# Performance work log

Hardware: AMD Instinct MI355X
Metric: run time of the kernel (lower is better)

The kernel has to match this reference:

```python
import jax, jax.numpy as jnp
from jax import lax
import numpy as np

D_MODEL = 1024
EXPAND = 2
D_INNER = D_MODEL * EXPAND
D_STATE = 16
D_CONV = 4
DECAY = 0.95
LN_EPS = 1e-5


def setup_inputs() -> dict:
    key = jax.random.key(0)
    ks = jax.random.split(key, 9)
    b, s = 4, 2048
    scale = 1.0 / np.sqrt(D_MODEL)
    inner_scale = 1.0 / np.sqrt(D_INNER)
    return {
        "x": jax.random.normal(ks[0], (b, s, D_MODEL), dtype=jnp.float32),
        "W_in": jax.random.normal(ks[1], (2 * D_INNER, D_MODEL), dtype=jnp.float32) * scale,
        "conv_w": jax.random.normal(ks[2], (D_INNER, 1, D_CONV), dtype=jnp.float32) * 0.5,
        "conv_b": jax.random.normal(ks[3], (D_INNER,), dtype=jnp.float32) * 0.1,
        "W_x": jax.random.normal(ks[4], (2 * D_STATE, D_INNER), dtype=jnp.float32) * inner_scale,
        "B_log": jax.random.normal(ks[5], (D_INNER, D_STATE), dtype=jnp.float32) * 0.05,  # xavier-ish small
        "W_out": jax.random.normal(ks[6], (D_MODEL, D_INNER), dtype=jnp.float32) * inner_scale,
        "ln_g": jnp.ones((D_MODEL,), dtype=jnp.float32),
        "ln_b": jnp.zeros((D_MODEL,), dtype=jnp.float32),
    }


def _ssm_block(x, W_in, conv_w, conv_b, W_x, B_log, W_out, ln_g, ln_b):
    b, s, _ = x.shape
    d_inner = W_in.shape[0] // 2
    d_conv = conv_w.shape[-1]

    # input projection and gate split
    xz = jnp.einsum('bsd,ed->bse', x, W_in)            # [b, s, 2*d_inner]
    x_inner, z = jnp.split(xz, 2, axis=-1)             # each [b, s, d_inner]

    # causal depthwise conv (left pad d_conv-1, output length s)
    xc = jnp.transpose(x_inner, (0, 2, 1))             # [b, d_inner, s]
    conv = lax.conv_general_dilated(
        xc, conv_w, window_strides=(1,), padding=[(d_conv - 1, 0)],
        feature_group_count=d_inner)
    conv = conv + conv_b[None, :, None]
    x_conv = jax.nn.silu(jnp.transpose(conv, (0, 2, 1)))  # [b, s, d_inner]

    # selective parameters; s_B is produced but unused in the original math
    sp = jnp.einsum('bsd,nd->bsn', x_conv, W_x)        # [b, s, 2*d_state]
    _s_B, s_C = jnp.split(sp, 2, axis=-1)              # each [b, s, d_state]

    B = jnp.exp(B_log)                                  # [d_inner, d_state]

    # state_t = 0.95*state_{t-1} + B * x_t  factorizes as  state = B[d,n]*h[b,t,d]
    # with h_t = 0.95*h_{t-1} + x_conv_t ; scan over time with [b, d_inner] carry.
    def step(h, xt):
        h = DECAY * h + xt
        return h, h

    h0 = jnp.zeros((b, d_inner), dtype=x.dtype)
    _, h = lax.scan(step, h0, jnp.swapaxes(x_conv, 0, 1))  # [s, b, d_inner]
    h = jnp.swapaxes(h, 0, 1)                              # [b, s, d_inner]

    # output_t[b,d] = sum_n state[b,d,n]*s_C[b,t,n] = h[b,t,d] * (s_C @ B^T)[b,t,d]
    y = h * jnp.einsum('bsn,dn->bsd', s_C, B)
    y = y * jax.nn.silu(z)
    y = jnp.einsum('bsd,od->bso', y, W_out)            # [b, s, d_model]

    resid = x + y
    mu = jnp.mean(resid, axis=-1, keepdims=True)
    var = jnp.var(resid, axis=-1, keepdims=True)
    return (resid - mu) * lax.rsqrt(var + LN_EPS) * ln_g + ln_b


def reference(x, W_in, conv_w, conv_b, W_x, B_log, W_out, ln_g, ln_b):
    return _ssm_block(x, W_in, conv_w, conv_b, W_x, B_log, W_out, ln_g, ln_b)
```

## Files before the change

### kernel.cpp

```cpp
#include <hip/hip_runtime.h>
#include <hip/hip_bf16.h>
#include <stdint.h>

#define DM   1024
#define DI   2048
#define NST  16
#define BSZ  4
#define SLEN 2048
#define MROWS (BSZ*SLEN)
#define CHUNK 32
#define NCH  (SLEN/CHUNK)
#define DECAYF 0.95f
#define MB (size_t)1048576

typedef _Float16 f16;
typedef __attribute__((ext_vector_type(2))) _Float16 f16x2;
typedef __attribute__((ext_vector_type(4))) _Float16 f16x4;
typedef __attribute__((ext_vector_type(8))) _Float16 f16x8;
typedef __attribute__((ext_vector_type(4))) float f32x4;

__device__ __forceinline__ float silu_f(float v) { return v / (1.f + __expf(-v)); }

__device__ __forceinline__ void gload16(const f16* lds, const f16* g) {
  __builtin_amdgcn_global_load_lds((const __attribute__((address_space(1))) void*)g,
                                   (__attribute__((address_space(3))) void*)lds, 16, 0, 0);
}

#define NX4  (MROWS * DM / 4)
#define NWI4 (2 * DI * DM / 4)
#define NWO4 (DM * DI / 4)
#define NWX4 (NST * DI / 4)
#define NE4  (NST * DI / 4)
__global__ __launch_bounds__(256) void cvt_all(
    const float* __restrict__ x, const float* __restrict__ wi, const float* __restrict__ wo,
    const float* __restrict__ Wx, const float* __restrict__ B_log,
    f16* __restrict__ A1, f16* __restrict__ B1, f16* __restrict__ W2,
    f16* __restrict__ WxC, f16* __restrict__ expBT)
{
  int i = blockIdx.x * 256 + threadIdx.x;
  if (i < NX4 + NWI4 + NWO4 + NWX4) {
    const float* src; f16* dst; int j;
    if (i < NX4)                     { src = x;  dst = A1; j = i; }
    else if (i < NX4 + NWI4)         { src = wi; dst = B1; j = i - NX4; }
    else if (i < NX4 + NWI4 + NWO4)  { src = wo; dst = W2; j = i - NX4 - NWI4; }
    else                             { src = Wx + (size_t)NST * DI; dst = WxC; j = i - NX4 - NWI4 - NWO4; }
    float4 v = ((const float4*)src)[j];
    f16x4 o = {(f16)v.x, (f16)v.y, (f16)v.z, (f16)v.w};
    ((f16x4*)dst)[j] = o;
  } else {
    int j = i - NX4 - NWI4 - NWO4 - NWX4;
    int base = j * 4;
    int n = base >> 11, d = base & (DI - 1);
    f16x4 o = {(f16)__expf(B_log[(d + 0) * NST + n]), (f16)__expf(B_log[(d + 1) * NST + n]),
               (f16)__expf(B_log[(d + 2) * NST + n]), (f16)__expf(B_log[(d + 3) * NST + n])};
    ((f16x4*)expBT)[j] = o;
  }
}

#define G1K 1024

__device__ __forceinline__ void stage_t(const f16* __restrict__ mat, int matBase,
                                        int kt, f16* ldsDst, int tid) {
  #pragma unroll
  for (int q = 0; q < 2; ++q) {
    int c = q * 512 + tid;
    int row = c >> 2, p = c & 3;
    int su = p ^ ((row >> 1) & 3);
    gload16(ldsDst + c * 8, mat + (size_t)(matBase + row) * G1K + kt * 32 + su * 8);
  }
}

#define WAITV(n) asm volatile("s_waitcnt vmcnt(" #n ")" ::: "memory")

__global__ __launch_bounds__(512, 2) void gemm1_8ph(
    const f16* __restrict__ A, const f16* __restrict__ Bt,
    f16* __restrict__ Xi, f16* __restrict__ Zs)
{
  __shared__ __align__(16) f16 lds[65536];
  const int tid  = threadIdx.x;
  const int lane = tid & 63;
  const int w    = tid >> 6;
  const int wr   = w >> 2, wc = w & 3;
  const int lr   = lane & 15;
  const int lq   = lane >> 4;

  const int nwg = gridDim.x * gridDim.y;
  int wgid = blockIdx.y * gridDim.x + blockIdx.x;
  wgid = (wgid & 7) * (nwg >> 3) + (wgid >> 3);
  const int bx = wgid % gridDim.x;
  const int by = wgid / gridDim.x;
  const int mBase = by * 256;
  const int nBase = bx * 256;

  f32x4 acc[8][4];
  #pragma unroll
  for (int mf = 0; mf < 8; ++mf)
    #pragma unroll
    for (int nf = 0; nf < 4; ++nf)
      acc[mf][nf] = (f32x4){0.f, 0.f, 0.f, 0.f};

  auto rdA = [&](int S, int mf) -> f16x8 {
    int ra = wr * 128 + mf * 16 + lr;
    return *(const f16x8*)&lds[S + ra * 32 + (lq ^ ((ra >> 1) & 3)) * 8];
  };
  auto rdB = [&](int S, int nf) -> f16x8 {
    int rb = wc * 64 + nf * 16 + lr;
    return *(const f16x8*)&lds[S + 8192 + rb * 32 + (lq ^ ((rb >> 1) & 3)) * 8];
  };

  f16x8 bfr[4], afr[8];

#define PH(S, ISSUE, TAIL) do {                                                 \
    _Pragma("unroll")                                                           \
    for (int nf = 0; nf < 4; ++nf) bfr[nf] = rdB((S), nf);                      \
    _Pragma("unroll")                                                           \
    for (int mm = 0; mm < 8; ++mm) afr[mm] = rdA((S), mm);                      \
    ISSUE;                                                                      \
    __builtin_amdgcn_s_barrier();                                               \
    asm volatile("s_waitcnt lgkmcnt(0)" ::: "memory");                          \
    __builtin_amdgcn_sched_barrier(0);                                          \
    __builtin_amdgcn_s_setprio(1);                                              \
    _Pragma("unroll")                                                           \
    for (int mm = 0; mm < 8; ++mm)                                              \
      _Pragma("unroll")                                                         \
      for (int nf = 0; nf < 4; ++nf)                                            \
        acc[mm][nf] = __builtin_amdgcn_mfma_f32_16x16x32_f16(                   \
            afr[mm], bfr[nf], acc[mm][nf], 0, 0, 0);                            \
    __builtin_amdgcn_s_setprio(0);                                              \
    __builtin_amdgcn_sched_barrier(0);                                          \
    TAIL;                                                                       \
    __builtin_amdgcn_s_barrier();                                               \
  } while (0)

  stage_t(A,  mBase, 0, &lds[0],             tid);
  stage_t(Bt, nBase, 0, &lds[8192],          tid);
  stage_t(A,  mBase, 1, &lds[16384],         tid);
  stage_t(Bt, nBase, 1, &lds[16384 + 8192],  tid);
  stage_t(A,  mBase, 2, &lds[32768],         tid);
  stage_t(Bt, nBase, 2, &lds[32768 + 8192],  tid);
  WAITV(8);
  __builtin_amdgcn_s_barrier();

  #pragma unroll
  for (int T = 0; T < 32; ++T) {
    const int S = (T & 3) * 16384;
    const int F = ((T + 3) & 3) * 16384;
    PH(S,
       { if (T + 3 < 32) { stage_t(A, mBase, T + 3, &lds[F], tid);
                           stage_t(Bt, nBase, T + 3, &lds[F + 8192], tid); } },
       { if (T < 29) { WAITV(8); } else if (T == 29) { WAITV(4); } else if (T == 30) { WAITV(0); } });
  }
#undef PH

  __syncthreads();
  const int rq = lq * 4;
  #pragma unroll
  for (int mf = 0; mf < 8; ++mf)
    #pragma unroll
    for (int nf = 0; nf < 4; ++nf)
      #pragma unroll
      for (int r = 0; r < 4; ++r)
        lds[(wr * 128 + mf * 16 + rq + r) * 256 + wc * 64 + nf * 16 + lr] = (f16)acc[mf][nf][r];
  __syncthreads();
  #pragma unroll
  for (int it = 0; it < 16; ++it) {
    int cidx = it * 512 + tid;
    int row = cidx >> 5;
    int col8 = (cidx & 31) * 8;
    int grow = mBase + row;
    int gcol = nBase + col8;
    f16x8 v = *(const f16x8*)&lds[row * 256 + col8];
    if (gcol < DI) *(f16x8*)&Xi[(size_t)grow * DI + gcol] = v;
    else           *(f16x8*)&Zs[(size_t)grow * DI + (gcol - DI)] = v;
  }
}

#define G2K 2048
#define SLOT2 12288

__device__ __forceinline__ void stage2_A(const f16* __restrict__ mat, int mBase,
                                         int kt, f16* ldsDst, int tid) {
  #pragma unroll
  for (int q = 0; q < 2; ++q) {
    int c = q * 512 + tid;
    int row = c >> 2, p = c & 3;
    int su = p ^ ((row >> 1) & 3);
    gload16(ldsDst + c * 8, mat + (size_t)(mBase + row) * G2K + kt * 32 + su * 8);
  }
}
__device__ __forceinline__ void stage2_B(const f16* __restrict__ mat, int nBase,
                                         int kt, f16* ldsDst, int tid) {
  int c = tid;
  int row = c >> 2, p = c & 3;
  int su = p ^ ((row >> 1) & 3);
  gload16(ldsDst + c * 8, mat + (size_t)(nBase + row) * G2K + kt * 32 + su * 8);
}

__global__ __launch_bounds__(512, 2) void gemm2_pipe(
    const f16* __restrict__ A, const f16* __restrict__ Bt, f16* __restrict__ G)
{
  __shared__ __align__(16) f16 lds[49152];
  const int tid  = threadIdx.x;
  const int lane = tid & 63;
  const int w    = tid >> 6;
  const int wr   = w >> 2, wc = w & 3;
  const int lr   = lane & 15;
  const int lq   = lane >> 4;

  const int nwg = gridDim.x * gridDim.y;
  int wgid = blockIdx.y * gridDim.x + blockIdx.x;
  wgid = (wgid & 7) * (nwg >> 3) + (wgid >> 3);
  const int bx = wgid % gridDim.x;
  const int by = wgid / gridDim.x;
  const int mBase = by * 256;
  const int nBase = bx * 128;

  f32x4 acc[8][2];
  #pragma unroll
  for (int mf = 0; mf < 8; ++mf)
    #pragma unroll
    for (int nf = 0; nf < 2; ++nf)
      acc[mf][nf] = (f32x4){0.f, 0.f, 0.f, 0.f};

  auto rdA = [&](int S, int mf) -> f16x8 {
    int ra = wr * 128 + mf * 16 + lr;
    return *(const f16x8*)&lds[S + ra * 32 + (lq ^ ((ra >> 1) & 3)) * 8];
  };
  auto rdB = [&](int S, int nf) -> f16x8 {
    int rb = wc * 32 + nf * 16 + lr;
    return *(const f16x8*)&lds[S + 8192 + rb * 32 + (lq ^ ((rb >> 1) & 3)) * 8];
  };

  f16x8 bfr[2], afr[8];

#define PH2(S, ISSUE, TAIL) do {                                                \
    _Pragma("unroll")                                                           \
    for (int nf = 0; nf < 2; ++nf) bfr[nf] = rdB((S), nf);                      \
    _Pragma("unroll")                                                           \
    for (int mm = 0; mm < 8; ++mm) afr[mm] = rdA((S), mm);                      \
    ISSUE;                                                                      \
    __builtin_amdgcn_s_barrier();                                               \
    asm volatile("s_waitcnt lgkmcnt(0)" ::: "memory");                          \
    __builtin_amdgcn_sched_barrier(0);                                          \
    __builtin_amdgcn_s_setprio(1);                                              \
    _Pragma("unroll")                                                           \
    for (int mm = 0; mm < 8; ++mm)                                              \
      _Pragma("unroll")                                                         \
      for (int nf = 0; nf < 2; ++nf)                                            \
        acc[mm][nf] = __builtin_amdgcn_mfma_f32_16x16x32_f16(                   \
            afr[mm], bfr[nf], acc[mm][nf], 0, 0, 0);                            \
    __builtin_amdgcn_s_setprio(0);                                              \
    __builtin_amdgcn_sched_barrier(0);                                          \
    TAIL;                                                                       \
    __builtin_amdgcn_s_barrier();                                               \
  } while (0)

  stage2_A(A,  mBase, 0, &lds[0],                 tid);
  stage2_B(Bt, nBase, 0, &lds[8192],              tid);
  stage2_A(A,  mBase, 1, &lds[SLOT2],             tid);
  stage2_B(Bt, nBase, 1, &lds[SLOT2 + 8192],      tid);
  stage2_A(A,  mBase, 2, &lds[2 * SLOT2],         tid);
  stage2_B(Bt, nBase, 2, &lds[2 * SLOT2 + 8192],  tid);
  WAITV(6);
  __builtin_amdgcn_s_barrier();

  #pragma unroll
  for (int T = 0; T < 64; ++T) {
    const int S = (T & 3) * SLOT2;
    const int F = ((T + 3) & 3) * SLOT2;
    PH2(S,
        { if (T + 3 < 64) { stage2_A(A, mBase, T + 3, &lds[F], tid);
                            stage2_B(Bt, nBase, T + 3, &lds[F + 8192], tid); } },
        { if (T < 61) { WAITV(6); } else if (T == 61) { WAITV(3); } else if (T == 62) { WAITV(0); } });
  }
#undef PH2

  __syncthreads();
  const int rq = lq * 4;
  #pragma unroll
  for (int mf = 0; mf < 8; ++mf)
    #pragma unroll
    for (int nf = 0; nf < 2; ++nf)
      #pragma unroll
      for (int r = 0; r < 4; ++r)
        lds[(wr * 128 + mf * 16 + rq + r) * 128 + wc * 32 + nf * 16 + lr] = (f16)acc[mf][nf][r];
  __syncthreads();
  #pragma unroll
  for (int it = 0; it < 8; ++it) {
    int cidx = it * 512 + tid;
    int row = cidx >> 4;
    int col8 = (cidx & 15) * 8;
    f16x8 v = *(const f16x8*)&lds[row * 128 + col8];
    *(f16x8*)&G[(size_t)(mBase + row) * DM + nBase + col8] = v;
  }
}

__global__ __launch_bounds__(256) void conv_scan(
    const f16* __restrict__ Xi, const float* __restrict__ convW, const float* __restrict__ convB,
    f16* __restrict__ Xc, f16* __restrict__ Hl, float* __restrict__ L)
{
  const int tid = threadIdx.x;
  const int d0 = tid * 8;
  const int ch = blockIdx.x;
  const int b  = blockIdx.y;
  const int t0 = ch * CHUNK;

  float w0[8], w1[8], w2[8], w3[8], cb[8];
  #pragma unroll
  for (int i = 0; i < 8; ++i) {
    float4 wv = ((const float4*)convW)[d0 + i];
    w0[i] = wv.x; w1[i] = wv.y; w2[i] = wv.z; w3[i] = wv.w;
    cb[i] = convB[d0 + i];
  }

  float xm3[8], xm2[8], xm1[8];
  auto loadrow = [&](int t, float* dst) {
    if (t < 0) {
      #pragma unroll
      for (int i = 0; i < 8; ++i) dst[i] = 0.f;
      return;
    }
    f16x8 v = *(const f16x8*)&Xi[((size_t)(b * SLEN + t)) * DI + d0];
    #pragma unroll
    for (int i = 0; i < 8; ++i) dst[i] = (float)v[i];
  };
  loadrow(t0 - 3, xm3); loadrow(t0 - 2, xm2); loadrow(t0 - 1, xm1);

  float h[8] = {0.f, 0.f, 0.f, 0.f, 0.f, 0.f, 0.f, 0.f};
  for (int t = 0; t < CHUNK; ++t) {
    const size_t ro = ((size_t)(b * SLEN + t0 + t)) * DI + d0;
    f16x8 xv = *(const f16x8*)&Xi[ro];
    f16x8 xco, hho;
    #pragma unroll
    for (int i = 0; i < 8; ++i) {
      float xt = (float)xv[i];
      float c = cb[i] + w0[i]*xm3[i] + w1[i]*xm2[i] + w2[i]*xm1[i] + w3[i]*xt;
      float xc = silu_f(c);
      h[i] = DECAYF * h[i] + xc;
      xco[i] = (f16)xc;
      hho[i] = (f16)h[i];
      xm3[i] = xm2[i]; xm2[i] = xm1[i]; xm1[i] = xt;
    }
    *(f16x8*)&Xc[ro] = xco;
    *(f16x8*)&Hl[ro] = hho;
  }
  const size_t lo = ((size_t)(b * NCH + ch)) * DI + d0;
  float4 l0 = {h[0], h[1], h[2], h[3]};
  float4 l1 = {h[4], h[5], h[6], h[7]};
  *(float4*)&L[lo] = l0;
  *(float4*)&L[lo + 4] = l1;
}

__global__ __launch_bounds__(256) void sc_carry(
    const f16* __restrict__ Xc, const f16* __restrict__ WxC, const float* __restrict__ L,
    float* __restrict__ sC, f16* __restrict__ Carry)
{
  const int tid = threadIdx.x;
  if (blockIdx.x >= 2048) {
    int i = (blockIdx.x - 2048) * 256 + tid;
    int b = i >> 11, d = i & (DI - 1);
    float dp = 1.f;
    #pragma unroll
    for (int k = 0; k < CHUNK; ++k) dp *= DECAYF;
    float c = 0.f;
    for (int ch0 = 0; ch0 < NCH; ch0 += 8) {
      float lv[8];
      #pragma unroll
      for (int k = 0; k < 8; ++k)
        lv[k] = L[((size_t)(b * NCH + ch0 + k)) * DI + d];
      #pragma unroll
      for (int k = 0; k < 8; ++k) {
        c = dp * c + lv[k];
        Carry[((size_t)(b * NCH + ch0 + k)) * DI + d] = (f16)c;
      }
    }
    return;
  }
  const int m = blockIdx.x * 4 + (tid >> 6);
  const int lane = tid & 63;
  float acc[16];
  #pragma unroll
  for (int n = 0; n < 16; ++n) acc[n] = 0.f;
  #pragma unroll
  for (int it = 0; it < DI / 512; ++it) {
    int d = it * 512 + lane * 8;
    f16x8 xv = *(const f16x8*)&Xc[(size_t)m * DI + d];
    #pragma unroll
    for (int n = 0; n < 16; ++n) {
      f16x8 wv = *(const f16x8*)&WxC[(size_t)n * DI + d];
      float s = 0.f;
      #pragma unroll
      for (int i = 0; i < 8; ++i) s += (float)xv[i] * (float)wv[i];
      acc[n] += s;
    }
  }
  #pragma unroll
  for (int n = 0; n < 16; ++n) {
    #pragma unroll
    for (int off = 32; off > 0; off >>= 1) acc[n] += __shfl_xor(acc[n], off);
  }
  if (lane == 0) {
    #pragma unroll
    for (int n = 0; n < 16; ++n) sC[m * 16 + n] = acc[n];
  }
}

__global__ __launch_bounds__(256) void ew_y(
    const f16* __restrict__ Hl, const f16* __restrict__ Zs,
    const float* __restrict__ sC, const f16* __restrict__ expBT,
    const f16* __restrict__ Carry, f16* __restrict__ Y)
{
  const int r = threadIdx.x >> 6, lane = threadIdx.x & 63;
  const int m = blockIdx.y * 4 + r;
  const int d0 = blockIdx.x * 512 + lane * 8;
  const int b = m >> 11, t = m & (SLEN - 1);
  const int ch = t / CHUNK, tl = t & (CHUNK - 1);

  float coef = 0.f;
  if (ch > 0) {
    coef = 1.f;
    for (int j = 0; j <= tl; ++j) coef *= DECAYF;
  }

  const float4 sc0 = *(const float4*)&sC[m * 16 + 0];
  const float4 sc1 = *(const float4*)&sC[m * 16 + 4];
  const float4 sc2 = *(const float4*)&sC[m * 16 + 8];
  const float4 sc3 = *(const float4*)&sC[m * 16 + 12];
  const float scv[16] = {sc0.x, sc0.y, sc0.z, sc0.w, sc1.x, sc1.y, sc1.z, sc1.w,
                         sc2.x, sc2.y, sc2.z, sc2.w, sc3.x, sc3.y, sc3.z, sc3.w};

  const size_t ro = (size_t)m * DI + d0;
  f16x8 hvv = *(const f16x8*)&Hl[ro];
  f16x8 zvv = *(const f16x8*)&Zs[ro];
  float hv[8], zv[8], ca[8];
  #pragma unroll
  for (int i = 0; i < 8; ++i) {
    hv[i] = (float)hvv[i];
    zv[i] = silu_f((float)zvv[i]);
    ca[i] = 0.f;
  }
  if (ch > 0) {
    const size_t co = ((size_t)(b * NCH + ch - 1)) * DI + d0;
    f16x8 cv = *(const f16x8*)&Carry[co];
    #pragma unroll
    for (int i = 0; i < 8; ++i) ca[i] = (float)cv[i];
  }

  float cp[8] = {0.f, 0.f, 0.f, 0.f, 0.f, 0.f, 0.f, 0.f};
  #pragma unroll
  for (int n = 0; n < 16; ++n) {
    f16x8 ev = *(const f16x8*)&expBT[(size_t)n * DI + d0];
    #pragma unroll
    for (int i = 0; i < 8; ++i) cp[i] += scv[n] * (float)ev[i];
  }

  f16x8 o;
  #pragma unroll
  for (int i = 0; i < 8; ++i) {
    float y = (hv[i] + coef * ca[i]) * cp[i] * zv[i];
    o[i] = (f16)y;
  }
  *(f16x8*)&Y[ro] = o;
}

__global__ __launch_bounds__(256) void ln_res(const f16* __restrict__ G, const float* __restrict__ x,
                                              const float* __restrict__ lng, const float* __restrict__ lnb,
                                              float* __restrict__ out) {
  const int m = blockIdx.x;
  const int tid = threadIdx.x;
  f16x4 gv4 = ((const f16x4*)(G + (size_t)m * DM))[tid];
  float4 xv = ((const float4*)(x + (size_t)m * DM))[tid];
  float4 rv = {(float)gv4.x + xv.x, (float)gv4.y + xv.y, (float)gv4.z + xv.z, (float)gv4.w + xv.w};
  float s = rv.x + rv.y + rv.z + rv.w;
  float s2 = rv.x * rv.x + rv.y * rv.y + rv.z * rv.z + rv.w * rv.w;
  #pragma unroll
  for (int off = 32; off > 0; off >>= 1) {
    s += __shfl_xor(s, off);
    s2 += __shfl_xor(s2, off);
  }
  __shared__ float ps[8];
  const int w = tid >> 6;
  if ((tid & 63) == 0) { ps[w] = s; ps[w + 4] = s2; }
  __syncthreads();
  float S = ps[0] + ps[1] + ps[2] + ps[3];
  float S2 = ps[4] + ps[5] + ps[6] + ps[7];
  float mu = S * (1.f / DM);
  float var = S2 * (1.f / DM) - mu * mu;
  float rs = rsqrtf(var + 1e-5f);
  float4 gg = ((const float4*)lng)[tid];
  float4 bb = ((const float4*)lnb)[tid];
  float4 ov = {(rv.x - mu) * rs * gg.x + bb.x, (rv.y - mu) * rs * gg.y + bb.y,
               (rv.z - mu) * rs * gg.z + bb.z, (rv.w - mu) * rs * gg.w + bb.w};
  ((float4*)(out + (size_t)m * DM))[tid] = ov;
}

extern "C" void kernel_launch(void* const* d_in, const int* in_sizes, int n_in,
                              void* d_out, int out_size, void* d_ws, size_t ws_size,
                              hipStream_t stream) {
  const float* x      = (const float*)d_in[0];
  const float* W_in   = (const float*)d_in[1];
  const float* conv_w = (const float*)d_in[2];
  const float* conv_b = (const float*)d_in[3];
  const float* W_x    = (const float*)d_in[4];
  const float* B_log  = (const float*)d_in[5];
  const float* W_out  = (const float*)d_in[6];
  const float* ln_g   = (const float*)d_in[7];
  const float* ln_b   = (const float*)d_in[8];
  float* out = (float*)d_out;

  char* ws = (char*)d_ws;
  f16*   Xi  = (f16*)(ws + 0);
  f16*   Yp  = (f16*)(ws + 0);
  f16*   Zs  = (f16*)(ws + 32 * MB);
  f16*   Xc  = (f16*)(ws + 64 * MB);
  f16*   Hl  = (f16*)(ws + 96 * MB);
  f16*   A1  = (f16*)(ws + 128 * MB);
  f16*   B1  = (f16*)(ws + 144 * MB);
  f16*   W2  = (f16*)(ws + 152 * MB);
  f16*   G   = (f16*)(ws + 156 * MB);
  float* L     = (float*)(ws + 172 * MB);
  f16*   Carry = (f16*)(ws + 174 * MB);
  float* sC    = (float*)(ws + 175 * MB);
  f16*   expBT = (f16*)(ws + 176 * MB);
  f16*   WxC   = (f16*)(ws + 177 * MB);

  cvt_all<<<(NX4 + NWI4 + NWO4 + NWX4 + NE4) / 256, 256, 0, stream>>>(
      x, W_in, W_out, W_x, B_log, A1, B1, W2, WxC, expBT);

  gemm1_8ph<<<dim3(2 * DI / 256, MROWS / 256), 512, 0, stream>>>(A1, B1, Xi, Zs);

  conv_scan<<<dim3(NCH, BSZ), 256, 0, stream>>>(Xi, conv_w, conv_b, Xc, Hl, L);
  sc_carry<<<2048 + 32, 256, 0, stream>>>(Xc, WxC, L, sC, Carry);
  ew_y<<<dim3(DI / 512, MROWS / 4), 256, 0, stream>>>(Hl, Zs, sC, expBT, Carry, Yp);

  gemm2_pipe<<<dim3(DM / 128, MROWS / 256), 512, 0, stream>>>(Yp, W2, G);

  ln_res<<<MROWS, 256, 0, stream>>>(G, x, ln_g, ln_b, out);
}
```

Before: 249.3 us.

## Fuse s_C projection into conv/scan kernel and drop Xc buffer

Computes the x_conv·W_x(C half) dot products inside the conv+scan kernel, reducing each row's 16 outputs with wave shuffles and shared memory, so x_conv is never written to or reread from global memory. The carry scan becomes its own small kernel. This removes the 32MB Xc write and the reread in sc_carry. In exchange the conv kernel, which has only 256 blocks, now does 16 shuffle reductions per timestep and holds more registers (16 f16x8 weight vectors), which may slow that serial-ish kernel.

```diff
diff --git a/kernel.cpp b/kernel.cpp
--- a/kernel.cpp
+++ b/kernel.cpp
@@ -295,12 +295,15 @@
   }
 }
 
-__global__ __launch_bounds__(256) void conv_scan(
+__global__ __launch_bounds__(256) void conv_sc(
     const f16* __restrict__ Xi, const float* __restrict__ convW, const float* __restrict__ convB,
-    f16* __restrict__ Xc, f16* __restrict__ Hl, float* __restrict__ L)
+    const f16* __restrict__ WxC,
+    f16* __restrict__ Hl, float* __restrict__ L, float* __restrict__ sC)
 {
+  __shared__ float red[CHUNK][4][16];
   const int tid = threadIdx.x;
   const int d0 = tid * 8;
+  const int wave = tid >> 6, lane = tid & 63;
   const int ch = blockIdx.x;
   const int b  = blockIdx.y;
   const int t0 = ch * CHUNK;
@@ -312,6 +315,9 @@
     w0[i] = wv.x; w1[i] = wv.y; w2[i] = wv.z; w3[i] = wv.w;
     cb[i] = convB[d0 + i];
   }
+  f16x8 wx[16];
+  #pragma unroll
+  for (int n = 0; n < 16; ++n) wx[n] = *(const f16x8*)&WxC[(size_t)n * DI + d0];
 
   float xm3[8], xm2[8], xm1[8];
   auto loadrow = [&](int t, float* dst) {
@@ -330,78 +336,69 @@
   for (int t = 0; t < CHUNK; ++t) {
     const size_t ro = ((size_t)(b * SLEN + t0 + t)) * DI + d0;
     f16x8 xv = *(const f16x8*)&Xi[ro];
-    f16x8 xco, hho;
+    f16x8 hho;
+    float xc[8];
     #pragma unroll
     for (int i = 0; i < 8; ++i) {
       float xt = (float)xv[i];
       float c = cb[i] + w0[i]*xm3[i] + w1[i]*xm2[i] + w2[i]*xm1[i] + w3[i]*xt;
-      float xc = silu_f(c);
-      h[i] = DECAYF * h[i] + xc;
-      xco[i] = (f16)xc;
+      xc[i] = silu_f(c);
+      h[i] = DECAYF * h[i] + xc[i];
       hho[i] = (f16)h[i];
       xm3[i] = xm2[i]; xm2[i] = xm1[i]; xm1[i] = xt;
     }
-    *(f16x8*)&Xc[ro] = xco;
     *(f16x8*)&Hl[ro] = hho;
+    float s[16];
+    #pragma unroll
+    for (int n = 0; n < 16; ++n) {
+      float v = 0.f;
+      #pragma unroll
+      for (int i = 0; i < 8; ++i) v += xc[i] * (float)wx[n][i];
+      s[n] = v;
+    }
+    #pragma unroll
+    for (int n = 0; n < 16; ++n) {
+      #pragma unroll
+      for (int off = 32; off > 0; off >>= 1) s[n] += __shfl_xor(s[n], off);
+    }
+    if (lane == 0) {
+      #pragma unroll
+      for (int n = 0; n < 16; ++n) red[t][wave][n] = s[n];
+    }
   }
   const size_t lo = ((size_t)(b * NCH + ch)) * DI + d0;
   float4 l0 = {h[0], h[1], h[2], h[3]};
   float4 l1 = {h[4], h[5], h[6], h[7]};
   *(float4*)&L[lo] = l0;
   *(float4*)&L[lo + 4] = l1;
-}
-
-__global__ __launch_bounds__(256) void sc_carry(
-    const f16* __restrict__ Xc, const f16* __restrict__ WxC, const float* __restrict__ L,
-    float* __restrict__ sC, f16* __restrict__ Carry)
-{
-  const int tid = threadIdx.x;
-  if (blockIdx.x >= 2048) {
-    int i = (blockIdx.x - 2048) * 256 + tid;
-    int b = i >> 11, d = i & (DI - 1);
-    float dp = 1.f;
-    #pragma unroll
-    for (int k = 0; k < CHUNK; ++k) dp *= DECAYF;
-    float c = 0.f;
-    for (int ch0 = 0; ch0 < NCH; ch0 += 8) {
-      float lv[8];
-      #pragma unroll
-      for (int k = 0; k < 8; ++k)
-        lv[k] = L[((size_t)(b * NCH + ch0 + k)) * DI + d];
-      #pragma unroll
-      for (int k = 0; k < 8; ++k) {
-        c = dp * c + lv[k];
-        Carry[((size_t)(b * NCH + ch0 + k)) * DI + d] = (f16)c;
-      }
+
+  __syncthreads();
+  #pragma unroll
+  for (int k = 0; k < 2; ++k) {
+    int idx = k * 256 + tid;
+    int t = idx >> 4, n = idx & 15;
+    float v = red[t][0][n] + red[t][1][n] + red[t][2][n] + red[t][3][n];
+    sC[((size_t)(b * SLEN + t0 + t)) * 16 + n] = v;
+  }
+}
+
+__global__ void carry_scan(const float* __restrict__ L, f16* __restrict__ Carry) {
+  int i = blockIdx.x * blockDim.x + threadIdx.x;
+  int b = i >> 11, d = i & (DI - 1);
+  float dp = 1.f;
+  #pragma unroll
+  for (int k = 0; k < CHUNK; ++k) dp *= DECAYF;
+  float c = 0.f;
+  for (int ch0 = 0; ch0 < NCH; ch0 += 8) {
+    float lv[8];
+    #pragma unroll
+    for (int k = 0; k < 8; ++k)
+      lv[k] = L[((size_t)(b * NCH + ch0 + k)) * DI + d];
+    #pragma unroll
+    for (int k = 0; k < 8; ++k) {
+      c = dp * c + lv[k];
+      Carry[((size_t)(b * NCH + ch0 + k)) * DI + d] = (f16)c;
     }
-    return;
-  }
-  const int m = blockIdx.x * 4 + (tid >> 6);
-  const int lane = tid & 63;
-  float acc[16];
-  #pragma unroll
-  for (int n = 0; n < 16; ++n) acc[n] = 0.f;
-  #pragma unroll
-  for (int it = 0; it < DI / 512; ++it) {
-    int d = it * 512 + lane * 8;
-    f16x8 xv = *(const f16x8*)&Xc[(size_t)m * DI + d];
-    #pragma unroll
-    for (int n = 0; n < 16; ++n) {
-      f16x8 wv = *(const f16x8*)&WxC[(size_t)n * DI + d];
-      float s = 0.f;
-      #pragma unroll
-      for (int i = 0; i < 8; ++i) s += (float)xv[i] * (float)wv[i];
-      acc[n] += s;
-    }
-  }
-  #pragma unroll
-  for (int n = 0; n < 16; ++n) {
-    #pragma unroll
-    for (int off = 32; off > 0; off >>= 1) acc[n] += __shfl_xor(acc[n], off);
-  }
-  if (lane == 0) {
-    #pragma unroll
-    for (int n = 0; n < 16; ++n) sC[m * 16 + n] = acc[n];
   }
 }
 
@@ -512,7 +509,6 @@
   f16*   Xi  = (f16*)(ws + 0);
   f16*   Yp  = (f16*)(ws + 0);
   f16*   Zs  = (f16*)(ws + 32 * MB);
-  f16*   Xc  = (f16*)(ws + 64 * MB);
   f16*   Hl  = (f16*)(ws + 96 * MB);
   f16*   A1  = (f16*)(ws + 128 * MB);
   f16*   B1  = (f16*)(ws + 144 * MB);
@@ -529,8 +525,8 @@
 
   gemm1_8ph<<<dim3(2 * DI / 256, MROWS / 256), 512, 0, stream>>>(A1, B1, Xi, Zs);
 
-  conv_scan<<<dim3(NCH, BSZ), 256, 0, stream>>>(Xi, conv_w, conv_b, Xc, Hl, L);
-  sc_carry<<<2048 + 32, 256, 0, stream>>>(Xc, WxC, L, sC, Carry);
+  conv_sc<<<dim3(NCH, BSZ), 256, 0, stream>>>(Xi, conv_w, conv_b, WxC, Hl, L, sC);
+  carry_scan<<<(BSZ * DI) / 256, 256, 0, stream>>>(L, Carry);
   ew_y<<<dim3(DI / 512, MROWS / 4), 256, 0, stream>>>(Hl, Zs, sC, expBT, Carry, Yp);
 
   gemm2_pipe<<<dim3(DM / 128, MROWS / 256), 512, 0, stream>>>(Yp, W2, G);
```

Measured after the change: 245.6 us. Within noise of the previous version (-1.5%).
